# Kernel tuning notes

Measured on AMD Instinct MI355X. Metric: run time of the kernel, lower is better.

## Reference

```python
import jax, jax.numpy as jnp
import numpy as np

DECAY = 0.99
EPS = 1e-05
THRESHOLD = 2.0
CODEBOOK_SIZE = 2048
DIM = 256


def setup_inputs() -> dict:
    key = jax.random.key(0)
    k1, k2, k3 = jax.random.split(key, 3)
    x = jax.random.normal(k1, (32, 1500, DIM), dtype=jnp.float32)
    # kaiming_uniform_ with a=0: bound = sqrt(6 / fan_in)
    bound = float(np.sqrt(6.0 / DIM))
    embed = jax.random.uniform(k2, (CODEBOOK_SIZE, DIM), dtype=jnp.float32,
                               minval=-bound, maxval=bound)
    # warm EMA state: positive cluster sizes, consistent embed_avg
    cluster_size = jax.random.uniform(k3, (CODEBOOK_SIZE,), dtype=jnp.float32,
                                      minval=0.0, maxval=200.0)
    embed_avg = embed * cluster_size[:, None]
    return {"x": x, "embed": embed, "cluster_size": cluster_size,
            "embed_avg": embed_avg}


def reference(x, embed, cluster_size, embed_avg):
    shape = x.shape
    K = embed.shape[0]
    xf = x.reshape(-1, shape[-1])                       # [N, D]

    # quantize: negative squared Euclidean distance, argmax == argmin dist
    x2 = jnp.sum(xf * xf, axis=1, keepdims=True)        # [N, 1]
    e2 = jnp.sum(embed * embed, axis=1)                 # [K]
    dist = -(x2 - 2.0 * (xf @ embed.T) + e2[None, :])   # [N, K]
    embed_ind = jnp.argmax(dist, axis=-1)               # [N]

    # dequantize (embedding gather)
    quantize = embed[embed_ind].reshape(shape)          # [B, T, D]

    # training-path EMA statistics (onehot.sum(0) and x.T @ onehot, as segment sums)
    counts = jax.ops.segment_sum(jnp.ones(xf.shape[0], dtype=x.dtype),
                                 embed_ind, num_segments=K)        # [K]
    embed_sum = jax.ops.segment_sum(xf, embed_ind, num_segments=K) # [K, D]

    new_cluster_size = cluster_size * DECAY + (1.0 - DECAY) * counts
    new_embed_avg = embed_avg * DECAY + (1.0 - DECAY) * embed_sum

    n = new_cluster_size.sum()
    smoothed = (new_cluster_size + EPS) / (n + K * EPS) * n
    embed_normalized = new_embed_avg / smoothed[:, None]

    # dead-code expiration: replace expired codes with random batch vectors
    expired = new_cluster_size < THRESHOLD
    perm = jax.random.permutation(jax.random.key(1), xf.shape[0])[:K]
    replacement = xf[perm]                              # [K, D]
    new_embed = jnp.where(expired[:, None], replacement, embed_normalized)

    codes = embed_ind.reshape(shape[:-1])               # [B, T]
    return quantize, codes, new_cluster_size, new_embed_avg, new_embed
```

## Files before the change

kernel.cpp:

```cpp
#include <hip/hip_runtime.h>
#include <hip/hip_bf16.h>
#include <stdint.h>
#include <math.h>

#define N_TOK 48000
#define DIMS  256
#define KCB   2048
#define WND 0.10f
#define BIAS 32.0f

typedef __attribute__((ext_vector_type(8))) short bf16x8;
typedef __attribute__((ext_vector_type(4))) float f32x4;
typedef __attribute__((ext_vector_type(8))) unsigned short u16x8;

__device__ __forceinline__ unsigned short bf16rn(float f) {
  uint32_t u = __float_as_uint(f);
  uint32_t r = (u + 0x7FFFu + ((u >> 16) & 1u)) >> 16;
  return (unsigned short)r;
}

__device__ __forceinline__ uint32_t max3u(uint32_t a, uint32_t b, uint32_t c) {
  uint32_t d; asm("v_max3_u32 %0, %1, %2, %3" : "=v"(d) : "v"(a), "v"(b), "v"(c));
  return d;
}
__device__ __forceinline__ uint32_t med3u(uint32_t a, uint32_t b, uint32_t c) {
  uint32_t d; asm("v_med3_u32 %0, %1, %2, %3" : "=v"(d) : "v"(a), "v"(b), "v"(c));
  return d;
}
__device__ __forceinline__ uint32_t min3u(uint32_t a, uint32_t b, uint32_t c) {
  uint32_t d; asm("v_min3_u32 %0, %1, %2, %3" : "=v"(d) : "v"(a), "v"(b), "v"(c));
  return d;
}

__device__ __forceinline__ uint32_t packBiased(float fb, uint32_t invIdx) {
  float c = fmaxf(fb, 0.0f);
  return (__float_as_uint(c) & ~0x7FFu) | invIdx;
}
__device__ __forceinline__ uint32_t packThrBiased(float fb) {
  float c = fmaxf(fb, 0.0f);
  return __float_as_uint(c) & ~0x7FFu;
}
__device__ __forceinline__ float unpackBiased(uint32_t u) {
  return __uint_as_float(u & ~0x7FFu);
}
__device__ __forceinline__ void ins3u(uint32_t& b, uint32_t& s, uint32_t& t, uint32_t v) {
  uint32_t b0 = b;
  b = max(b, v);
  t = max(t, min3u(b0, s, v));
  s = med3u(b0, s, v);
}

__device__ inline void tf2x32(uint32_t k0, uint32_t k1, uint32_t c0, uint32_t c1,
                              uint32_t& o0, uint32_t& o1) {
  uint32_t ks2 = k0 ^ k1 ^ 0x1BD11BDAu;
  uint32_t x0 = c0 + k0, x1 = c1 + k1;
#define TF_R(r) { x0 += x1; x1 = (x1 << (r)) | (x1 >> (32 - (r))); x1 ^= x0; }
  TF_R(13) TF_R(15) TF_R(26) TF_R(6)
  x0 += k1; x1 += ks2 + 1u;
  TF_R(17) TF_R(29) TF_R(16) TF_R(24)
  x0 += ks2; x1 += k0 + 2u;
  TF_R(13) TF_R(15) TF_R(26) TF_R(6)
  x0 += k0; x1 += k1 + 3u;
  TF_R(17) TF_R(29) TF_R(16) TF_R(24)
  x0 += k1; x1 += ks2 + 4u;
  TF_R(13) TF_R(15) TF_R(26) TF_R(6)
  x0 += ks2; x1 += k0 + 5u;
#undef TF_R
  o0 = x0; o1 = x1;
}

__device__ inline void get_round_key(int round, uint32_t& ka, uint32_t& kb) {
  const uint32_t b0 = 0u, b1 = 1u;
  uint32_t K1a, K1b, S1a, S1b;
  tf2x32(b0, b1, 0u, 0u, K1a, K1b);
  tf2x32(b0, b1, 0u, 1u, S1a, S1b);
  if (round == 1) { ka = S1a; kb = S1b; return; }
  uint32_t S2a, S2b;
  tf2x32(K1a, K1b, 0u, 1u, S2a, S2b);
  ka = S2a; kb = S2b;
}

__device__ inline uint32_t gen_key(int round, uint32_t i) {
  uint32_t ka, kb, o0, o1;
  get_round_key(round, ka, kb);
  tf2x32(ka, kb, 0u, i, o0, o1);
  return o0 ^ o1;
}

__device__ __forceinline__ void gload_lds16(const void* g, void* l) {
  __builtin_amdgcn_global_load_lds(
      (const __attribute__((address_space(1))) uint32_t*)g,
      (__attribute__((address_space(3))) uint32_t*)l, 16, 0, 0);
}

__global__ void e2split_keys(const float* __restrict__ x, unsigned short* __restrict__ xh,
                             const float* __restrict__ embed, unsigned short* __restrict__ eh,
                             float* __restrict__ e2f, double* __restrict__ e2d,
                             uint32_t* __restrict__ keys1, uint32_t* __restrict__ keys2,
                             uint32_t* __restrict__ bcount1, uint32_t* __restrict__ bcount2) {
  const int nx = N_TOK * DIMS / 8;
  const int ne = KCB * DIMS / 8;
  int i = blockIdx.x * blockDim.x + threadIdx.x;
  if (i < nx + ne) {
    const float* src; unsigned short* dst; int j;
    if (i < nx) { src = x; dst = xh; j = i; }
    else { src = embed; dst = eh; j = i - nx; }
    float4 a = ((const float4*)src)[j * 2];
    float4 b = ((const float4*)src)[j * 2 + 1];
    float v[8] = {a.x, a.y, a.z, a.w, b.x, b.y, b.z, b.w};
    u16x8 h;
#pragma unroll
    for (int q = 0; q < 8; ++q) h[q] = bf16rn(v[q]);
    *(u16x8*)&dst[(size_t)j * 8] = h;
    return;
  }
  int k = i - (nx + ne);
  if (k < KCB) {
    const float4* er = (const float4*)(embed + (size_t)k * DIMS);
    float s = 0.f;
    double sd = 0.0;
    for (int c = 0; c < DIMS / 4; ++c) {
      float4 v = er[c];
      s = fmaf(v.x, v.x, s); s = fmaf(v.y, v.y, s);
      s = fmaf(v.z, v.z, s); s = fmaf(v.w, v.w, s);
      sd += (double)v.x * v.x + (double)v.y * v.y
          + (double)v.z * v.z + (double)v.w * v.w;
    }
    e2f[k] = BIAS - s;
    e2d[k] = sd;
    return;
  }
  int n = k - KCB;
  if (n < N_TOK) {
    uint32_t k1 = gen_key(1, (uint32_t)n);
    uint32_t k2 = gen_key(2, (uint32_t)n);
    keys1[n] = k1; keys2[n] = k2;
    atomicAdd(&bcount1[k1 >> 21], 1u);
    atomicAdd(&bcount2[k2 >> 21], 1u);
  }
}

__global__ __launch_bounds__(256, 2) void dist_mfma(
    const unsigned short* __restrict__ xh, const unsigned short* __restrict__ eh,
    const float* __restrict__ e2f,
    uint32_t* __restrict__ pb, uint32_t* __restrict__ ps, uint32_t* __restrict__ pt)
{
  __shared__ __align__(16) char smem[50688];
  short (*As)[128 * 32] = (short(*)[128 * 32])smem;
  short (*Bs)[256 * 32] = (short(*)[256 * 32])(smem + 16384);
  uint32_t* red = (uint32_t*)smem;

  const int tid = threadIdx.x;
  const int lane = tid & 63, w = tid >> 6;
  const int wr = w >> 1, wc = w & 1;
  const int l15 = lane & 15, lg = lane >> 4;

  int bx, by;
  {
    const int bid = blockIdx.x;
    if (bid < 2944) { int g = bid >> 6, r = bid & 63; bx = g * 8 + (r & 7); by = r >> 3; }
    else            { int t2 = bid - 2944; bx = 368 + (t2 % 7); by = t2 / 7; }
  }
  const int n0 = bx * 128;
  const int c0 = by * 256;

  f32x4 acc[4][8];
#pragma unroll
  for (int mf = 0; mf < 4; ++mf)
#pragma unroll
    for (int nf = 0; nf < 8; ++nf) acc[mf][nf] = (f32x4){0.f, 0.f, 0.f, 0.f};

  auto stage = [&](int t) {
    const int d0 = t << 5;
    const int q = t & 1;
#pragma unroll
    for (int i = 0; i < 2; ++i) {
      const int c = i * 256 + tid;
      const int row = c >> 2;
      const int sc = ((c & 3) ^ ((row >> 1) & 3)) << 3;
      gload_lds16(xh + (size_t)(n0 + row) * DIMS + d0 + sc, (void*)&As[q][c * 8]);
    }
#pragma unroll
    for (int i = 0; i < 4; ++i) {
      const int c = i * 256 + tid;
      const int row = c >> 2;
      const int sc = ((c & 3) ^ ((row >> 1) & 3)) << 3;
      gload_lds16(eh + (size_t)(c0 + row) * DIMS + d0 + sc, (void*)&Bs[q][c * 8]);
    }
  };

  stage(0);
  __syncthreads();

#pragma unroll 1
  for (int t = 0; t < 8; ++t) {
    if (t < 7) stage(t + 1);
    const int q = t & 1;
    bf16x8 af[4], bfv[8];
#pragma unroll
    for (int mf = 0; mf < 4; ++mf) {
      const int r = wr * 64 + mf * 16 + l15;
      af[mf] = *(const bf16x8*)&As[q][r * 32 + ((lg ^ ((r >> 1) & 3)) << 3)];
    }
#pragma unroll
    for (int nf = 0; nf < 8; ++nf) {
      const int r = wc * 128 + nf * 16 + l15;
      bfv[nf] = *(const bf16x8*)&Bs[q][r * 32 + ((lg ^ ((r >> 1) & 3)) << 3)];
    }
#pragma unroll
    for (int mf = 0; mf < 4; ++mf)
#pragma unroll
      for (int nf = 0; nf < 8; ++nf)
        acc[mf][nf] = __builtin_amdgcn_mfma_f32_16x16x32_bf16(
            af[mf], bfv[nf], acc[mf][nf], 0, 0, 0);
    __syncthreads();
  }

  float e2v[8];
  uint32_t inv[8];
#pragma unroll
  for (int nf = 0; nf < 8; ++nf) {
    int k = c0 + wc * 128 + nf * 16 + l15;
    e2v[nf] = e2f[k];
    inv[nf] = 2047u - (uint32_t)k;
  }

  const int colbase = wc * 16 + l15;
#pragma unroll
  for (int mf = 0; mf < 4; ++mf) {
#pragma unroll
    for (int reg = 0; reg < 4; ++reg) {
      uint32_t p0 = packBiased(fmaf(2.f, acc[mf][0][reg], e2v[0]), inv[0]);
      uint32_t p1 = packBiased(fmaf(2.f, acc[mf][1][reg], e2v[1]), inv[1]);
      uint32_t p2 = packBiased(fmaf(2.f, acc[mf][2][reg], e2v[2]), inv[2]);
      uint32_t b  = max3u(p0, p1, p2);
      uint32_t s  = med3u(p0, p1, p2);
      uint32_t t3 = min3u(p0, p1, p2);
#pragma unroll
      for (int nf = 3; nf < 8; ++nf) {
        float f = fmaf(2.f, acc[mf][nf][reg], e2v[nf]);
        ins3u(b, s, t3, packBiased(f, inv[nf]));
      }
      const int row = wr * 64 + mf * 16 + lg * 4 + reg;
      uint32_t* p = &red[row * 99 + colbase * 3];
      p[0] = b; p[1] = s; p[2] = t3;
    }
  }
  __syncthreads();
  {
    const int row = tid >> 1, half = tid & 1;
    uint32_t b = 0u, s = 0u, t3 = 0u;
    const uint32_t* p = &red[row * 99 + half * 48];
#pragma unroll 4
    for (int c = 0; c < 48; ++c) ins3u(b, s, t3, p[c]);
    if (half) {
      uint32_t* q = &red[row * 99 + 96];
      q[0] = b; q[1] = s; q[2] = t3;
    }
    __syncthreads();
    if (!half) {
      const uint32_t* q = &red[row * 99 + 96];
      ins3u(b, s, t3, q[0]);
      ins3u(b, s, t3, q[1]);
      ins3u(b, s, t3, q[2]);
      size_t o = (size_t)by * N_TOK + n0 + row;
      pb[o] = b; ps[o] = s; pt[o] = t3;
    }
  }
}

__global__ void merge8(const uint32_t* __restrict__ pb, const uint32_t* __restrict__ ps,
                       const uint32_t* __restrict__ pt,
                       int* __restrict__ ind,
                       int* __restrict__ candRows, int* __restrict__ candIdx,
                       int* __restrict__ candCnt, int* __restrict__ listC,
                       uint32_t* __restrict__ cntA, uint32_t* __restrict__ cntC,
                       float* __restrict__ outcodes, uint32_t* __restrict__ cntTok) {
  int n = blockIdx.x * blockDim.x + threadIdx.x;
  if (n >= N_TOK) return;
  uint32_t tb[8], tsv[8], ttv[8];
#pragma unroll
  for (int tt = 0; tt < 8; ++tt) {
    size_t o = (size_t)tt * N_TOK + n;
    tb[tt] = pb[o]; tsv[tt] = ps[o]; ttv[tt] = pt[o];
  }
  uint32_t best = tb[0];
#pragma unroll
  for (int tt = 1; tt < 8; ++tt) best = max(best, tb[tt]);
  int kb = 2047 - (int)(best & 0x7FFu);
  ind[n] = kb;
  const uint32_t thr = packThrBiased(unpackBiased(best) - WND);
  int m = 0; bool full = false;
#pragma unroll
  for (int tt = 0; tt < 8; ++tt) {
    m += (tb[tt] >= thr) + (tsv[tt] >= thr);
    full = full || (ttv[tt] >= thr);
  }
  if (full) {
    listC[atomicAdd(cntC, 1u)] = n;
  } else if (m > 1) {
    uint32_t i = atomicAdd(cntA, 1u);
    candRows[i] = n; candCnt[i] = m;
    int j = 0;
#pragma unroll
    for (int tt = 0; tt < 8; ++tt) {
      if (tb[tt]  >= thr) candIdx[(size_t)i * 16 + (j++)] = 2047 - (int)(tb[tt]  & 0x7FFu);
      if (tsv[tt] >= thr) candIdx[(size_t)i * 16 + (j++)] = 2047 - (int)(tsv[tt] & 0x7FFu);
    }
  } else {
    outcodes[n] = (float)kb;
    atomicAdd(&cntTok[kb], 1u);
  }
}

#define RC_BLOCKS 512
#define RF_BLOCKS 1024
__global__ void refine_both(const float* __restrict__ x, const float* __restrict__ embed,
                            const double* __restrict__ e2d,
                            const int* __restrict__ candRows, const int* __restrict__ candIdx,
                            const int* __restrict__ candCnt,
                            const int* __restrict__ listC,
                            const uint32_t* __restrict__ cntAB,
                            int* __restrict__ ind,
                            float* __restrict__ outcodes, uint32_t* __restrict__ cntTok) {
  __shared__ double xd[DIMS];
  __shared__ double rv[256];
  __shared__ int    rk[256];
  const int tid = threadIdx.x;
  if (blockIdx.x < RC_BLOCKS) {
    const uint32_t nA = cntAB[0];
    const int lane = tid & 63;
    const uint32_t wid = ((uint32_t)blockIdx.x * 256 + tid) >> 6;
    const uint32_t nw = RC_BLOCKS * 4;
    for (uint32_t i = wid; i < nA; i += nw) {
      const int n = candRows[i];
      const int m = candCnt[i];
      float4 xv = ((const float4*)x)[(size_t)n * 64 + lane];
      double best = -1e300; int bk = 0x7fffffff;
      for (int j = 0; j < m; ++j) {
        int k = candIdx[(size_t)i * 16 + j];
        float4 e4 = ((const float4*)embed)[(size_t)k * 64 + lane];
        double d = (double)xv.x * e4.x + (double)xv.y * e4.y
                 + (double)xv.z * e4.z + (double)xv.w * e4.w;
#pragma unroll
        for (int mm = 1; mm < 64; mm <<= 1) d += __shfl_xor(d, mm);
        double v = 2.0 * d - e2d[k];
        if (v > best || (v == best && k < bk)) { best = v; bk = k; }
      }
      if (lane == 0) {
        ind[n] = bk;
        outcodes[n] = (float)bk;
        atomicAdd(&cntTok[bk], 1u);
      }
    }
    return;
  }
  const uint32_t nC = cntAB[1];
  for (uint32_t it = blockIdx.x - RC_BLOCKS; it < nC; it += RF_BLOCKS) {
    const int n = listC[it];
    __syncthreads();
    xd[tid] = (double)x[(size_t)n * DIMS + tid];
    __syncthreads();
    double best = -1e300; int bk = 0x7fffffff;
    for (int k = tid; k < KCB; k += 256) {
      const float4* er = (const float4*)(embed + (size_t)k * DIMS);
      double a0 = 0.0, a1 = 0.0, a2 = 0.0, a3 = 0.0;
      for (int c = 0; c < 64; c += 4) {
        float4 ea = er[c], eb = er[c + 1], ec = er[c + 2], ed = er[c + 3];
        int d = c * 4;
        a0 += xd[d + 0] * ea.x + xd[d + 1] * ea.y + xd[d + 2] * ea.z + xd[d + 3] * ea.w;
        a1 += xd[d + 4] * eb.x + xd[d + 5] * eb.y + xd[d + 6] * eb.z + xd[d + 7] * eb.w;
        a2 += xd[d + 8] * ec.x + xd[d + 9] * ec.y + xd[d + 10] * ec.z + xd[d + 11] * ec.w;
        a3 += xd[d + 12] * ed.x + xd[d + 13] * ed.y + xd[d + 14] * ed.z + xd[d + 15] * ed.w;
      }
      double v = 2.0 * (a0 + a1 + a2 + a3) - e2d[k];
      if (v > best || (v == best && k < bk)) { best = v; bk = k; }
    }
    rv[tid] = best; rk[tid] = bk;
    __syncthreads();
    for (int s = 128; s > 0; s >>= 1) {
      if (tid < s) {
        double v2 = rv[tid + s]; int k2 = rk[tid + s];
        if (v2 > rv[tid] || (v2 == rv[tid] && k2 < rk[tid])) { rv[tid] = v2; rk[tid] = k2; }
      }
      __syncthreads();
    }
    if (tid == 0) {
      ind[n] = rk[0];
      outcodes[n] = (float)rk[0];
      atomicAdd(&cntTok[rk[0]], 1u);
    }
  }
}

__global__ void gather_scan(const float* __restrict__ embed, const int* __restrict__ ind,
                            float* __restrict__ outq,
                            const uint32_t* __restrict__ cntTok, uint32_t* __restrict__ tokBase,
                            uint32_t* __restrict__ tokCur,
                            const float* __restrict__ cs, float* __restrict__ out_ncs,
                            int* __restrict__ expired, double* __restrict__ nsum,
                            const uint32_t* __restrict__ bcount1, uint32_t* __restrict__ bbase1,
                            uint32_t* __restrict__ cursor1,
                            const uint32_t* __restrict__ bcount2, uint32_t* __restrict__ bbase2,
                            uint32_t* __restrict__ cursor2) {
  __shared__ uint32_t buf[2][2048];
  __shared__ double sd[1024];
  const int t = threadIdx.x;
  if (blockIdx.x >= 3) {
    int idx = (blockIdx.x - 3) * 1024 + t;
    if (idx < N_TOK * 64) {
      int n = idx >> 6, c = idx & 63;
      ((float4*)outq)[idx] = ((const float4*)embed)[(size_t)ind[n] * 64 + c];
    }
    return;
  }
  const uint32_t* in; uint32_t* out; uint32_t* cz;
  if (blockIdx.x == 0)      { in = cntTok;  out = tokBase; cz = tokCur;  }
  else if (blockIdx.x == 1) { in = bcount1; out = bbase1;  cz = cursor1; }
  else                      { in = bcount2; out = bbase2;  cz = cursor2; }
  double local = 0.0;
  for (int q = 0; q < 2; ++q) {
    int i = t + q * 1024;
    uint32_t c = in[i];
    buf[0][i] = c;
    cz[i] = 0;
    if (blockIdx.x == 0) {
      double v = 0.99 * (double)cs[i] + 0.01 * (double)c;
      out_ncs[i] = (float)v;
      expired[i] = (v < 2.0) ? 1 : 0;
      local += v;
    }
  }
  if (blockIdx.x == 0) sd[t] = local;
  __syncthreads();
  int src = 0;
  for (int off = 1; off < 2048; off <<= 1) {
    for (int q = 0; q < 2; ++q) {
      int i = t + q * 1024;
      uint32_t v = buf[src][i];
      if (i >= off) v += buf[src][i - off];
      buf[src ^ 1][i] = v;
    }
    src ^= 1; __syncthreads();
  }
  for (int q = 0; q < 2; ++q) {
    int i = t + q * 1024;
    out[i] = buf[src][i] - in[i];
  }
  if (blockIdx.x == 0) {
    for (int s = 512; s > 0; s >>= 1) { if (t < s) sd[t] += sd[t + s]; __syncthreads(); }
    if (t == 0) nsum[0] = sd[0];
  }
}

__global__ void scatter_both(const int* __restrict__ ind, const uint32_t* __restrict__ tokBase,
                             uint32_t* __restrict__ tokCur, uint32_t* __restrict__ tokBucket,
                             const uint32_t* __restrict__ keys1, const uint32_t* __restrict__ bbase1,
                             uint32_t* __restrict__ cursor1,
                             uint32_t* __restrict__ bkey, uint32_t* __restrict__ bval) {
  int n = blockIdx.x * blockDim.x + threadIdx.x;
  if (n >= N_TOK) return;
  int k = ind[n];
  uint32_t p = atomicAdd(&tokCur[k], 1u);
  tokBucket[tokBase[k] + p] = (uint32_t)n;
  uint32_t k1 = keys1[n];
  uint32_t b = k1 >> 21;
  uint32_t q = atomicAdd(&cursor1[b], 1u);
  uint32_t s = bbase1[b] + q;
  bkey[s] = k1; bval[s] = (uint32_t)n;
}

#define ES_BLOCKS 512
__global__ void esum_rank1(const float* __restrict__ x, const uint32_t* __restrict__ tokBase,
                           const uint32_t* __restrict__ cntTok,
                           const uint32_t* __restrict__ tokBucket,
                           float* __restrict__ esum,
                           const uint32_t* __restrict__ bkey, const uint32_t* __restrict__ bval,
                           const uint32_t* __restrict__ bbase1, const uint32_t* __restrict__ bcount1,
                           const uint32_t* __restrict__ keys2,
                           const uint32_t* __restrict__ bbase2, uint32_t* __restrict__ cursor2,
                           uint32_t* __restrict__ bkey2, uint32_t* __restrict__ bval2,
                           uint32_t* __restrict__ bpos2) {
  const int tid = threadIdx.x;
  if (blockIdx.x < ES_BLOCKS) {
    const uint32_t wv = ((uint32_t)blockIdx.x * 256 + tid) >> 6;
    const int lane = tid & 63;
    const uint32_t base = tokBase[wv], cnt = cntTok[wv];
    float4 a0 = {0.f, 0.f, 0.f, 0.f}, a1 = {0.f, 0.f, 0.f, 0.f};
    uint32_t i = 0;
    for (; i + 2 <= cnt; i += 2) {
      uint32_t n0 = tokBucket[base + i], n1 = tokBucket[base + i + 1];
      float4 v0 = ((const float4*)x)[(size_t)n0 * 64 + lane];
      float4 v1 = ((const float4*)x)[(size_t)n1 * 64 + lane];
      a0.x += v0.x; a0.y += v0.y; a0.z += v0.z; a0.w += v0.w;
      a1.x += v1.x; a1.y += v1.y; a1.z += v1.z; a1.w += v1.w;
    }
    if (i < cnt) {
      uint32_t n0 = tokBucket[base + i];
      float4 v0 = ((const float4*)x)[(size_t)n0 * 64 + lane];
      a0.x += v0.x; a0.y += v0.y; a0.z += v0.z; a0.w += v0.w;
    }
    float4 r; r.x = a0.x + a1.x; r.y = a0.y + a1.y; r.z = a0.z + a1.z; r.w = a0.w + a1.w;
    ((float4*)esum)[(size_t)wv * 64 + lane] = r;
    return;
  }
  int b = blockIdx.x - ES_BLOCKS;
  uint32_t base = bbase1[b], cnt = bcount1[b];
  for (uint32_t t = tid; t < cnt; t += 256) {
    uint32_t k = bkey[base + t], pv = bval[base + t];
    uint32_t r = 0;
    for (uint32_t j = 0; j < cnt; ++j) {
      uint32_t kj = bkey[base + j], pj = bval[base + j];
      r += (kj < k) | ((kj == k) & (pj < pv));
    }
    uint32_t p = base + r;
    uint32_t k2 = keys2[p];
    uint32_t b2 = k2 >> 21;
    uint32_t q = atomicAdd(&cursor2[b2], 1u);
    uint32_t s = bbase2[b2] + q;
    bkey2[s] = k2; bval2[s] = pv; bpos2[s] = p;
  }
}

__global__ void rank2(const uint32_t* __restrict__ bkey2, const uint32_t* __restrict__ bval2,
                      const uint32_t* __restrict__ bpos2,
                      const uint32_t* __restrict__ bbase2, const uint32_t* __restrict__ bcount2,
                      uint32_t* __restrict__ perm) {
  int b = blockIdx.x;
  uint32_t base = bbase2[b];
  if (base >= KCB) return;
  uint32_t cnt = bcount2[b];
  for (uint32_t t = threadIdx.x; t < cnt; t += blockDim.x) {
    uint32_t k = bkey2[base + t], p = bpos2[base + t];
    uint32_t r = 0;
    for (uint32_t j = 0; j < cnt; ++j) {
      uint32_t kj = bkey2[base + j], pj = bpos2[base + j];
      r += (kj < k) | ((kj == k) & (pj < p));
    }
    uint32_t pos = base + r;
    if (pos < KCB) perm[pos] = bval2[base + t];
  }
}

__global__ void final_embed(const float* __restrict__ x, const float* __restrict__ cs,
                            const uint32_t* __restrict__ cntTok,
                            const float* __restrict__ eavg, const float* __restrict__ esum,
                            const int* __restrict__ expired, const double* __restrict__ nsum,
                            const uint32_t* __restrict__ perm,
                            float* __restrict__ out_eavg, float* __restrict__ out_ne) {
  int idx = blockIdx.x * blockDim.x + threadIdx.x;
  if (idx >= KCB * 64) return;
  int k = idx >> 6, c = idx & 63;
  float4 ea = ((const float4*)eavg)[idx];
  float4 es = ((const float4*)esum)[idx];
  double ax = 0.99 * (double)ea.x + 0.01 * (double)es.x;
  double ay = 0.99 * (double)ea.y + 0.01 * (double)es.y;
  double az = 0.99 * (double)ea.z + 0.01 * (double)es.z;
  double aw = 0.99 * (double)ea.w + 0.01 * (double)es.w;
  float4 nv; nv.x = (float)ax; nv.y = (float)ay; nv.z = (float)az; nv.w = (float)aw;
  ((float4*)out_eavg)[idx] = nv;
  float4 r;
  if (expired[k]) {
    r = ((const float4*)x)[(size_t)perm[k] * 64 + c];
  } else {
    double ncs = 0.99 * (double)cs[k] + 0.01 * (double)cntTok[k];
    double n = nsum[0];
    double sm = (ncs + 1e-5) / (n + 2048.0 * 1e-5) * n;
    r.x = (float)(ax / sm); r.y = (float)(ay / sm);
    r.z = (float)(az / sm); r.w = (float)(aw / sm);
  }
  ((float4*)out_ne)[idx] = r;
}

extern "C" void kernel_launch(void* const* d_in, const int* in_sizes, int n_in,
                              void* d_out, int out_size, void* d_ws, size_t ws_size,
                              hipStream_t stream) {
  const float* x     = (const float*)d_in[0];
  const float* embed = (const float*)d_in[1];
  const float* cs    = (const float*)d_in[2];
  const float* eavg  = (const float*)d_in[3];

  float* out = (float*)d_out;
  float* outQ    = out;
  float* outC    = out + 12288000;
  float* outNCS  = out + 12336000;
  float* outEAVG = out + 12338048;
  float* outNE   = out + 12862336;

  char* w = (char*)d_ws;
  size_t off = 0;
  auto alloc = [&](size_t bytes) -> void* {
    void* p = w + off; off += (bytes + 255) & ~(size_t)255; return p;
  };
  unsigned short* xh = (unsigned short*)alloc((size_t)N_TOK * DIMS * 2);
  unsigned short* eh = (unsigned short*)alloc((size_t)KCB * DIMS * 2);
  float*    e2f     = (float*)alloc(KCB * 4);
  double*   e2d     = (double*)alloc(KCB * 8);
  float*    esum    = (float*)alloc((size_t)KCB * DIMS * 4);
  uint32_t* pbest   = (uint32_t*)alloc((size_t)8 * N_TOK * 4);
  uint32_t* psecond = (uint32_t*)alloc((size_t)8 * N_TOK * 4);
  uint32_t* pthird  = (uint32_t*)alloc((size_t)8 * N_TOK * 4);
  int*      ind     = (int*)alloc(N_TOK * 4);
  int*      candRows= (int*)alloc(N_TOK * 4);
  int*      candCnt = (int*)alloc(N_TOK * 4);
  int*      candIdx = (int*)alloc((size_t)N_TOK * 16 * 4);
  int*      listC   = (int*)alloc(N_TOK * 4);
  double*   nsum    = (double*)alloc(256);
  int*      expired = (int*)alloc(KCB * 4);
  uint32_t* tokBase = (uint32_t*)alloc(KCB * 4);
  uint32_t* tokCur  = (uint32_t*)alloc(KCB * 4);
  uint32_t* tokBucket = (uint32_t*)alloc(N_TOK * 4);
  uint32_t* keys1   = (uint32_t*)alloc(N_TOK * 4);
  uint32_t* keys2   = (uint32_t*)alloc(N_TOK * 4);
  uint32_t* bkey    = (uint32_t*)alloc(N_TOK * 4);
  uint32_t* bval    = (uint32_t*)alloc(N_TOK * 4);
  uint32_t* bkey2   = (uint32_t*)alloc(N_TOK * 4);
  uint32_t* bval2   = (uint32_t*)alloc(N_TOK * 4);
  uint32_t* bpos2   = (uint32_t*)alloc(N_TOK * 4);
  uint32_t* bbase1  = (uint32_t*)alloc(KCB * 4);
  uint32_t* bbase2  = (uint32_t*)alloc(KCB * 4);
  uint32_t* cursor1 = (uint32_t*)alloc(KCB * 4);
  uint32_t* cursor2 = (uint32_t*)alloc(KCB * 4);
  uint32_t* perm    = (uint32_t*)alloc(KCB * 4);
  uint32_t* cntAB   = (uint32_t*)alloc(256);
  uint32_t* cntTok  = (uint32_t*)alloc(KCB * 4);
  uint32_t* bcount1 = (uint32_t*)alloc(KCB * 4);
  uint32_t* bcount2 = (uint32_t*)alloc(KCB * 4);

  hipMemsetAsync(cntAB, 0, 256 + 3 * KCB * 4, stream);

  e2split_keys<<<(N_TOK * DIMS / 8 + KCB * DIMS / 8 + KCB + N_TOK + 255) / 256, 256, 0,
                 stream>>>(x, xh, embed, eh, e2f, e2d, keys1, keys2, bcount1, bcount2);

  dist_mfma<<<3000, 256, 0, stream>>>(xh, eh, e2f, pbest, psecond, pthird);
  merge8<<<188, 256, 0, stream>>>(pbest, psecond, pthird,
                                  ind, candRows, candIdx, candCnt, listC,
                                  &cntAB[0], &cntAB[1], outC, cntTok);
  refine_both<<<RC_BLOCKS + RF_BLOCKS, 256, 0, stream>>>(
      x, embed, e2d, candRows, candIdx, candCnt, listC, cntAB, ind, outC, cntTok);

  gather_scan<<<3 + (N_TOK * 64 + 1023) / 1024, 1024, 0, stream>>>(
      embed, ind, outQ,
      cntTok, tokBase, tokCur, cs, outNCS, expired, nsum,
      bcount1, bbase1, cursor1, bcount2, bbase2, cursor2);
  scatter_both<<<188, 256, 0, stream>>>(ind, tokBase, tokCur, tokBucket,
                                        keys1, bbase1, cursor1, bkey, bval);
  esum_rank1<<<ES_BLOCKS + KCB, 256, 0, stream>>>(
      x, tokBase, cntTok, tokBucket, esum,
      bkey, bval, bbase1, bcount1, keys2, bbase2, cursor2, bkey2, bval2, bpos2);
  rank2<<<2048, 64, 0, stream>>>(bkey2, bval2, bpos2, bbase2, bcount2, perm);

  final_embed<<<512, 256, 0, stream>>>(x, cs, cntTok, eavg, esum, expired, nsum,
                                       perm, outEAVG, outNE);
}
```

Measured before the change: 226.3 us.

## Fold memset into prep kernel, pad LDS rows, bf16 esum, fuse perm gather

Replaces the hipMemsetAsync with zeroing inside the first kernel, and moves the bucket-count atomics into merge8. Pads the LDS reduction stride from 99 to 100 so the reduction can use 16-byte vector reads. Makes esum read the bf16 copy of x instead of fp32, halving gather traffic but lowering the precision of embed_sum and new_embed_avg. Has rank2 write expired replacement rows directly, which removes the perm buffer and the conditional gather in final_embed.

```diff
diff --git a/kernel.cpp b/kernel.cpp
--- a/kernel.cpp
+++ b/kernel.cpp
@@ -17,6 +17,9 @@
   uint32_t u = __float_as_uint(f);
   uint32_t r = (u + 0x7FFFu + ((u >> 16) & 1u)) >> 16;
   return (unsigned short)r;
+}
+__device__ __forceinline__ float bf16f(unsigned short h) {
+  return __uint_as_float(((uint32_t)h) << 16);
 }
 
 __device__ __forceinline__ uint32_t max3u(uint32_t a, uint32_t b, uint32_t c) {
@@ -93,11 +96,12 @@
       (__attribute__((address_space(3))) uint32_t*)l, 16, 0, 0);
 }
 
+#define NZERO 6208
 __global__ void e2split_keys(const float* __restrict__ x, unsigned short* __restrict__ xh,
                              const float* __restrict__ embed, unsigned short* __restrict__ eh,
                              float* __restrict__ e2f, double* __restrict__ e2d,
                              uint32_t* __restrict__ keys1, uint32_t* __restrict__ keys2,
-                             uint32_t* __restrict__ bcount1, uint32_t* __restrict__ bcount2) {
+                             uint32_t* __restrict__ zeroBase) {
   const int nx = N_TOK * DIMS / 8;
   const int ne = KCB * DIMS / 8;
   int i = blockIdx.x * blockDim.x + threadIdx.x;
@@ -132,12 +136,12 @@
   }
   int n = k - KCB;
   if (n < N_TOK) {
-    uint32_t k1 = gen_key(1, (uint32_t)n);
-    uint32_t k2 = gen_key(2, (uint32_t)n);
-    keys1[n] = k1; keys2[n] = k2;
-    atomicAdd(&bcount1[k1 >> 21], 1u);
-    atomicAdd(&bcount2[k2 >> 21], 1u);
-  }
+    keys1[n] = gen_key(1, (uint32_t)n);
+    keys2[n] = gen_key(2, (uint32_t)n);
+    return;
+  }
+  int z = n - N_TOK;
+  if (z < NZERO) zeroBase[z] = 0u;
 }
 
 __global__ __launch_bounds__(256, 2) void dist_mfma(
@@ -145,7 +149,7 @@
     const float* __restrict__ e2f,
     uint32_t* __restrict__ pb, uint32_t* __restrict__ ps, uint32_t* __restrict__ pt)
 {
-  __shared__ __align__(16) char smem[50688];
+  __shared__ __align__(16) char smem[51200];
   short (*As)[128 * 32] = (short(*)[128 * 32])smem;
   short (*Bs)[256 * 32] = (short(*)[256 * 32])(smem + 16384);
   uint32_t* red = (uint32_t*)smem;
@@ -242,7 +246,7 @@
         ins3u(b, s, t3, packBiased(f, inv[nf]));
       }
       const int row = wr * 64 + mf * 16 + lg * 4 + reg;
-      uint32_t* p = &red[row * 99 + colbase * 3];
+      uint32_t* p = &red[row * 100 + colbase * 3];
       p[0] = b; p[1] = s; p[2] = t3;
     }
   }
@@ -250,16 +254,20 @@
   {
     const int row = tid >> 1, half = tid & 1;
     uint32_t b = 0u, s = 0u, t3 = 0u;
-    const uint32_t* p = &red[row * 99 + half * 48];
-#pragma unroll 4
-    for (int c = 0; c < 48; ++c) ins3u(b, s, t3, p[c]);
+    const uint4* p4 = (const uint4*)&red[row * 100 + half * 48];
+#pragma unroll
+    for (int c = 0; c < 12; ++c) {
+      uint4 v = p4[c];
+      ins3u(b, s, t3, v.x); ins3u(b, s, t3, v.y);
+      ins3u(b, s, t3, v.z); ins3u(b, s, t3, v.w);
+    }
     if (half) {
-      uint32_t* q = &red[row * 99 + 96];
+      uint32_t* q = &red[row * 100 + 96];
       q[0] = b; q[1] = s; q[2] = t3;
     }
     __syncthreads();
     if (!half) {
-      const uint32_t* q = &red[row * 99 + 96];
+      const uint32_t* q = &red[row * 100 + 96];
       ins3u(b, s, t3, q[0]);
       ins3u(b, s, t3, q[1]);
       ins3u(b, s, t3, q[2]);
@@ -275,9 +283,13 @@
                        int* __restrict__ candRows, int* __restrict__ candIdx,
                        int* __restrict__ candCnt, int* __restrict__ listC,
                        uint32_t* __restrict__ cntA, uint32_t* __restrict__ cntC,
-                       float* __restrict__ outcodes, uint32_t* __restrict__ cntTok) {
+                       float* __restrict__ outcodes, uint32_t* __restrict__ cntTok,
+                       const uint32_t* __restrict__ keys1, const uint32_t* __restrict__ keys2,
+                       uint32_t* __restrict__ bcount1, uint32_t* __restrict__ bcount2) {
   int n = blockIdx.x * blockDim.x + threadIdx.x;
   if (n >= N_TOK) return;
+  atomicAdd(&bcount1[keys1[n] >> 21], 1u);
+  atomicAdd(&bcount2[keys2[n] >> 21], 1u);
   uint32_t tb[8], tsv[8], ttv[8];
 #pragma unroll
   for (int tt = 0; tt < 8; ++tt) {
@@ -471,7 +483,7 @@
 }
 
 #define ES_BLOCKS 512
-__global__ void esum_rank1(const float* __restrict__ x, const uint32_t* __restrict__ tokBase,
+__global__ void esum_rank1(const unsigned short* __restrict__ xh, const uint32_t* __restrict__ tokBase,
                            const uint32_t* __restrict__ cntTok,
                            const uint32_t* __restrict__ tokBucket,
                            float* __restrict__ esum,
@@ -490,15 +502,15 @@
     uint32_t i = 0;
     for (; i + 2 <= cnt; i += 2) {
       uint32_t n0 = tokBucket[base + i], n1 = tokBucket[base + i + 1];
-      float4 v0 = ((const float4*)x)[(size_t)n0 * 64 + lane];
-      float4 v1 = ((const float4*)x)[(size_t)n1 * 64 + lane];
-      a0.x += v0.x; a0.y += v0.y; a0.z += v0.z; a0.w += v0.w;
-      a1.x += v1.x; a1.y += v1.y; a1.z += v1.z; a1.w += v1.w;
+      ushort4 h0 = ((const ushort4*)xh)[(size_t)n0 * 64 + lane];
+      ushort4 h1 = ((const ushort4*)xh)[(size_t)n1 * 64 + lane];
+      a0.x += bf16f(h0.x); a0.y += bf16f(h0.y); a0.z += bf16f(h0.z); a0.w += bf16f(h0.w);
+      a1.x += bf16f(h1.x); a1.y += bf16f(h1.y); a1.z += bf16f(h1.z); a1.w += bf16f(h1.w);
     }
     if (i < cnt) {
       uint32_t n0 = tokBucket[base + i];
-      float4 v0 = ((const float4*)x)[(size_t)n0 * 64 + lane];
-      a0.x += v0.x; a0.y += v0.y; a0.z += v0.z; a0.w += v0.w;
+      ushort4 h0 = ((const ushort4*)xh)[(size_t)n0 * 64 + lane];
+      a0.x += bf16f(h0.x); a0.y += bf16f(h0.y); a0.z += bf16f(h0.z); a0.w += bf16f(h0.w);
     }
     float4 r; r.x = a0.x + a1.x; r.y = a0.y + a1.y; r.z = a0.z + a1.z; r.w = a0.w + a1.w;
     ((float4*)esum)[(size_t)wv * 64 + lane] = r;
@@ -525,7 +537,8 @@
 __global__ void rank2(const uint32_t* __restrict__ bkey2, const uint32_t* __restrict__ bval2,
                       const uint32_t* __restrict__ bpos2,
                       const uint32_t* __restrict__ bbase2, const uint32_t* __restrict__ bcount2,
-                      uint32_t* __restrict__ perm) {
+                      const int* __restrict__ expired, const float* __restrict__ x,
+                      float* __restrict__ out_ne) {
   int b = blockIdx.x;
   uint32_t base = bbase2[b];
   if (base >= KCB) return;
@@ -538,19 +551,23 @@
       r += (kj < k) | ((kj == k) & (pj < p));
     }
     uint32_t pos = base + r;
-    if (pos < KCB) perm[pos] = bval2[base + t];
-  }
-}
-
-__global__ void final_embed(const float* __restrict__ x, const float* __restrict__ cs,
+    if (pos < KCB && expired[pos]) {
+      uint32_t val = bval2[base + t];
+      const float4* src = (const float4*)x + (size_t)val * 64;
+      float4* dst = (float4*)out_ne + (size_t)pos * 64;
+      for (int c = 0; c < 64; ++c) dst[c] = src[c];
+    }
+  }
+}
+
+__global__ void final_embed(const float* __restrict__ cs,
                             const uint32_t* __restrict__ cntTok,
                             const float* __restrict__ eavg, const float* __restrict__ esum,
                             const int* __restrict__ expired, const double* __restrict__ nsum,
-                            const uint32_t* __restrict__ perm,
                             float* __restrict__ out_eavg, float* __restrict__ out_ne) {
   int idx = blockIdx.x * blockDim.x + threadIdx.x;
   if (idx >= KCB * 64) return;
-  int k = idx >> 6, c = idx & 63;
+  int k = idx >> 6;
   float4 ea = ((const float4*)eavg)[idx];
   float4 es = ((const float4*)esum)[idx];
   double ax = 0.99 * (double)ea.x + 0.01 * (double)es.x;
@@ -559,17 +576,15 @@
   double aw = 0.99 * (double)ea.w + 0.01 * (double)es.w;
   float4 nv; nv.x = (float)ax; nv.y = (float)ay; nv.z = (float)az; nv.w = (float)aw;
   ((float4*)out_eavg)[idx] = nv;
-  float4 r;
-  if (expired[k]) {
-    r = ((const float4*)x)[(size_t)perm[k] * 64 + c];
-  } else {
+  if (!expired[k]) {
     double ncs = 0.99 * (double)cs[k] + 0.01 * (double)cntTok[k];
     double n = nsum[0];
     double sm = (ncs + 1e-5) / (n + 2048.0 * 1e-5) * n;
+    float4 r;
     r.x = (float)(ax / sm); r.y = (float)(ay / sm);
     r.z = (float)(az / sm); r.w = (float)(aw / sm);
-  }
-  ((float4*)out_ne)[idx] = r;
+    ((float4*)out_ne)[idx] = r;
+  }
 }
 
 extern "C" void kernel_launch(void* const* d_in, const int* in_sizes, int n_in,
@@ -621,21 +636,19 @@
   uint32_t* bbase2  = (uint32_t*)alloc(KCB * 4);
   uint32_t* cursor1 = (uint32_t*)alloc(KCB * 4);
   uint32_t* cursor2 = (uint32_t*)alloc(KCB * 4);
-  uint32_t* perm    = (uint32_t*)alloc(KCB * 4);
   uint32_t* cntAB   = (uint32_t*)alloc(256);
   uint32_t* cntTok  = (uint32_t*)alloc(KCB * 4);
   uint32_t* bcount1 = (uint32_t*)alloc(KCB * 4);
   uint32_t* bcount2 = (uint32_t*)alloc(KCB * 4);
 
-  hipMemsetAsync(cntAB, 0, 256 + 3 * KCB * 4, stream);
-
-  e2split_keys<<<(N_TOK * DIMS / 8 + KCB * DIMS / 8 + KCB + N_TOK + 255) / 256, 256, 0,
-                 stream>>>(x, xh, embed, eh, e2f, e2d, keys1, keys2, bcount1, bcount2);
+  e2split_keys<<<(N_TOK * DIMS / 8 + KCB * DIMS / 8 + KCB + N_TOK + NZERO + 255) / 256,
+                 256, 0, stream>>>(x, xh, embed, eh, e2f, e2d, keys1, keys2, cntAB);
 
   dist_mfma<<<3000, 256, 0, stream>>>(xh, eh, e2f, pbest, psecond, pthird);
   merge8<<<188, 256, 0, stream>>>(pbest, psecond, pthird,
                                   ind, candRows, candIdx, candCnt, listC,
-                                  &cntAB[0], &cntAB[1], outC, cntTok);
+                                  &cntAB[0], &cntAB[1], outC, cntTok,
+                                  keys1, keys2, bcount1, bcount2);
   refine_both<<<RC_BLOCKS + RF_BLOCKS, 256, 0, stream>>>(
       x, embed, e2d, candRows, candIdx, candCnt, listC, cntAB, ind, outC, cntTok);
 
@@ -646,10 +659,11 @@
   scatter_both<<<188, 256, 0, stream>>>(ind, tokBase, tokCur, tokBucket,
                                         keys1, bbase1, cursor1, bkey, bval);
   esum_rank1<<<ES_BLOCKS + KCB, 256, 0, stream>>>(
-      x, tokBase, cntTok, tokBucket, esum,
+      xh, tokBase, cntTok, tokBucket, esum,
       bkey, bval, bbase1, bcount1, keys2, bbase2, cursor2, bkey2, bval2, bpos2);
-  rank2<<<2048, 64, 0, stream>>>(bkey2, bval2, bpos2, bbase2, bcount2, perm);
-
-  final_embed<<<512, 256, 0, stream>>>(x, cs, cntTok, eavg, esum, expired, nsum,
-                                       perm, outEAVG, outNE);
-}
+  rank2<<<2048, 64, 0, stream>>>(bkey2, bval2, bpos2, bbase2, bcount2,
+                                 expired, x, outNE);
+
+  final_embed<<<512, 256, 0, stream>>>(cs, cntTok, eavg, esum, expired, nsum,
+                                       outEAVG, outNE);
+}
```

After: 222.0 us. No clear change (-1.9%).
